# Optimization experiments

Measured on AMD Instinct MI355X. Metric: run time of the kernel, lower is better.

The kernel has to match this reference:

```python
import jax, jax.numpy as jnp
import numpy as np

EPS = 1e-5

def bn(x, g, b, m, v):
    # inference-mode BatchNorm2d over channel dim
    return (x - m[None, :, None, None]) * jax.lax.rsqrt(v[None, :, None, None] + EPS) * g[None, :, None, None] + b[None, :, None, None]

def conv1x1(x, W, b=None):
    y = jnp.einsum('oc,bchw->bohw', W, x)
    return y + b[None, :, None, None] if b is not None else y

def forward(x, W3, b3, g1, b1, m1, v1, Wa, ba, g2, b2, m2, v2, Wq, bq, Wk, bk, Wv, bv, gam, Wg, bg, g3, b3n, m3, v3, Wf, bf, g4, b4, m4, v4, Wr, rs):
    B, C, H, Wd = x.shape
    N = H * Wd
    # conv branch: 3x3 conv + BN + ReLU
    y3 = jax.lax.conv_general_dilated(x, W3, (1, 1), ((1, 1), (1, 1)), dimension_numbers=('NCHW', 'OIHW', 'NCHW'))
    local = jax.nn.relu(bn(y3 + b3[None, :, None, None], g1, b1, m1, v1))
    # attn branch: 1x1 conv + BN + ReLU, then full-resolution attention
    a = jax.nn.relu(bn(conv1x1(x, Wa, ba), g2, b2, m2, v2))
    q = conv1x1(a, Wq, bq).reshape(B, -1, N)   # [B, C/8, N]
    k = conv1x1(a, Wk, bk).reshape(B, -1, N)   # [B, C/8, N]
    v = conv1x1(a, Wv, bv).reshape(B, -1, N)   # [B, C, N]
    att = jax.nn.softmax(jnp.einsum('bcn,bcm->bnm', q, k), axis=-1)  # [B, N, N], unscaled as in source
    o = jnp.einsum('bcm,bnm->bcn', v, att).reshape(a.shape)
    attn_feat = gam * o + a
    # gated fusion
    combined = jnp.concatenate([local, attn_feat], axis=1)
    gate = jax.nn.sigmoid(bn(conv1x1(combined, Wg, bg), g3, b3n, m3, v3))
    fused = gate * local + (1.0 - gate) * attn_feat
    out = jax.nn.relu(bn(conv1x1(jnp.concatenate([fused, combined], axis=1), Wf, bf), g4, b4, m4, v4))
    res = conv1x1(x, Wr)  # residual 1x1 conv, no bias (in != out channels)
    return out + rs * res

def setup_inputs() -> dict:
    B, Ci, Co, H, W_ = 4, 64, 128, 64, 64
    Cq = Co // 8
    ks = jax.random.split(jax.random.key(0), 24)
    def rn(i, s, sc=0.05):
        return jax.random.normal(ks[i], s, jnp.float32) * sc
    def var(i, c):
        return jax.random.uniform(ks[i], (c,), jnp.float32, 0.5, 1.5)
    ones = lambda c: jnp.ones((c,), jnp.float32)
    zeros = lambda c: jnp.zeros((c,), jnp.float32)
    return {
        'x': rn(0, (B, Ci, H, W_), 1.0),
        'W3': rn(1, (Co, Ci, 3, 3)), 'b3': rn(2, (Co,)),
        'g1': ones(Co), 'b1': zeros(Co), 'm1': rn(3, (Co,), 0.1), 'v1': var(4, Co),
        'Wa': rn(5, (Co, Ci)), 'ba': rn(6, (Co,)),
        'g2': ones(Co), 'b2': zeros(Co), 'm2': rn(7, (Co,), 0.1), 'v2': var(8, Co),
        'Wq': rn(9, (Cq, Co)), 'bq': rn(10, (Cq,)),
        'Wk': rn(11, (Cq, Co)), 'bk': rn(12, (Cq,)),
        'Wv': rn(13, (Co, Co)), 'bv': rn(14, (Co,)),
        'gam': jnp.array(0.5, jnp.float32),
        'Wg': rn(15, (Co, 2 * Co)), 'bg': rn(16, (Co,)),
        'g3': ones(Co), 'b3n': zeros(Co), 'm3': rn(17, (Co,), 0.1), 'v3': var(18, Co),
        'Wf': rn(19, (Co, 3 * Co)), 'bf': rn(20, (Co,)),
        'g4': ones(Co), 'b4': zeros(Co), 'm4': rn(21, (Co,), 0.1), 'v4': var(22, Co),
        'Wr': rn(23, (Co, Ci)),
        'rs': jnp.array(0.1, jnp.float32),
    }

def reference(x, W3, b3, g1, b1, m1, v1, Wa, ba, g2, b2, m2, v2, Wq, bq, Wk, bk, Wv, bv, gam, Wg, bg, g3, b3n, m3, v3, Wf, bf, g4, b4, m4, v4, Wr, rs):
    return forward(x, W3, b3, g1, b1, m1, v1, Wa, ba, g2, b2, m2, v2, Wq, bq, Wk, bk, Wv, bv, gam, Wg, bg, g3, b3n, m3, v3, Wf, bf, g4, b4, m4, v4, Wr, rs)
```

## Files before the change

kernel.cpp:

```cpp
#include <hip/hip_runtime.h>
#include <hip/hip_bf16.h>

#define CI_ 64
#define CO_ 128
#define NPIX 4096
#define CQ_ 16
#define EPS_ 1e-5f

typedef __attribute__((ext_vector_type(8))) __bf16 bf16x8;
typedef __attribute__((ext_vector_type(4))) __bf16 bf16x4;
typedef __attribute__((ext_vector_type(4))) float f32x4;

__global__ __launch_bounds__(256) void z_prepx(
    const float* __restrict__ x, __bf16* __restrict__ xT)
{
    __shared__ float tl[64][65];
    int b = blockIdx.x >> 6;
    int n0 = (blockIdx.x & 63) * 64;
    int tid = threadIdx.x;
    int nn = tid & 63, c4 = tid >> 6;
#pragma unroll
    for (int p = 0; p < 16; ++p) {
        int ci = p * 4 + c4;
        tl[ci][nn] = x[((size_t)b * CI_ + ci) * NPIX + n0 + nn];
    }
    __syncthreads();
#pragma unroll
    for (int p = 0; p < 2; ++p) {
        int idx = p * 256 + tid;
        int n = idx >> 3, cig = idx & 7;
        bf16x8 vv;
#pragma unroll
        for (int j = 0; j < 8; ++j) vv[j] = (__bf16)tl[cig * 8 + j][n];
        ((bf16x8*)xT)[((size_t)b * NPIX + n0 + n) * 8 + cig] = vv;
    }
}

__global__ __launch_bounds__(256) void z_prepw2(
    const float* __restrict__ W3, __bf16* __restrict__ Wt2,
    const float* __restrict__ Wg, const float* __restrict__ Wf, const float* __restrict__ Wr,
    const float* __restrict__ Wa, const float* __restrict__ Wq, const float* __restrict__ Wk,
    const float* __restrict__ Wv, __bf16* __restrict__ Wb)
{
    int i = blockIdx.x * 256 + threadIdx.x;
    if (i < 73728) {
        int co = i / 576;
        int r = i - co * 576;
        int tap = r >> 6;
        int ci = r & 63;
        Wt2[i] = (__bf16)W3[((size_t)co * CI_ + ci) * 9 + tap];
    }
    if (i < 118784) {
        float val;
        if (i < 32768) val = Wg[i];
        else if (i < 81920) val = Wf[i - 32768];
        else if (i < 90112) val = Wr[i - 81920];
        else if (i < 98304) val = Wa[i - 90112];
        else if (i < 100352) val = Wq[i - 98304];
        else if (i < 102400) val = Wk[i - 100352];
        else val = Wv[i - 102400];
        Wb[i] = (__bf16)val;
    }
}

__global__ __launch_bounds__(256) void z_mega(
    const __bf16* __restrict__ xT, const __bf16* __restrict__ Wb,
    const float* __restrict__ ba, const float* __restrict__ g2, const float* __restrict__ b2,
    const float* __restrict__ m2, const float* __restrict__ v2,
    const float* __restrict__ bq, const float* __restrict__ bk, const float* __restrict__ bv,
    float* __restrict__ a, __bf16* __restrict__ qT, __bf16* __restrict__ kT, __bf16* __restrict__ V2)
{
    __shared__ __align__(16) __bf16 an[16 * 128];
    int tid = threadIdx.x;
    int b = blockIdx.x >> 8;
    int n0 = (blockIdx.x & 255) * 16;
    int l = tid & 63, w = tid >> 6;
    int lm = l & 15, g = l >> 4;

    const __bf16* Wa2 = Wb + 90112;
    const __bf16* Wq2 = Wb + 98304;
    const __bf16* Wk2 = Wb + 100352;
    const __bf16* Wv2 = Wb + 102400;

    bf16x8 bx[2];
#pragma unroll
    for (int kc = 0; kc < 2; ++kc)
        bx[kc] = ((const bf16x8*)xT)[((size_t)b * NPIX + n0 + lm) * 8 + (kc * 4 + g)];
    f32x4 pa[2];
#pragma unroll
    for (int ct = 0; ct < 2; ++ct) {
#pragma unroll
        for (int r = 0; r < 4; ++r) pa[ct][r] = ba[w * 32 + ct * 16 + g * 4 + r];
#pragma unroll
        for (int kc = 0; kc < 2; ++kc) {
            bf16x8 afr = *(const bf16x8*)&Wa2[(size_t)(w * 32 + ct * 16 + lm) * 64 + kc * 32 + g * 8];
            pa[ct] = __builtin_amdgcn_mfma_f32_16x16x32_bf16(afr, bx[kc], pa[ct], 0, 0, 0);
        }
    }
#pragma unroll
    for (int ct = 0; ct < 2; ++ct) {
        bf16x4 pk;
#pragma unroll
        for (int r = 0; r < 4; ++r) {
            int co = w * 32 + ct * 16 + g * 4 + r;
            float sc = rsqrtf(v2[co] + EPS_) * g2[co];
            float sh = b2[co] - m2[co] * sc;
            float y = fmaxf(pa[ct][r] * sc + sh, 0.f);
            a[((size_t)b * CO_ + co) * NPIX + n0 + lm] = y;
            pk[r] = (__bf16)y;
        }
        int co8 = w * 4 + ct * 2 + (g >> 1);
        int ch = co8 ^ (lm & 7);
        *(bf16x4*)&an[lm * 128 + ch * 8 + (g & 1) * 4] = pk;
    }
    __syncthreads();

    bf16x8 bn[4];
#pragma unroll
    for (int kc = 0; kc < 4; ++kc) {
        int ch = (kc * 4 + g) ^ (lm & 7);
        bn[kc] = *(const bf16x8*)&an[lm * 128 + ch * 8];
    }
    f32x4 pv[2];
#pragma unroll
    for (int ct = 0; ct < 2; ++ct) {
#pragma unroll
        for (int r = 0; r < 4; ++r) pv[ct][r] = bv[w * 32 + ct * 16 + g * 4 + r];
#pragma unroll
        for (int kc = 0; kc < 4; ++kc) {
            bf16x8 afr = *(const bf16x8*)&Wv2[(size_t)(w * 32 + ct * 16 + lm) * 128 + kc * 32 + g * 8];
            pv[ct] = __builtin_amdgcn_mfma_f32_16x16x32_bf16(afr, bn[kc], pv[ct], 0, 0, 0);
        }
    }
    int n = n0 + lm;
#pragma unroll
    for (int ct = 0; ct < 2; ++ct)
#pragma unroll
        for (int r = 0; r < 4; ++r) {
            int c = w * 32 + ct * 16 + g * 4 + r;
            V2[(size_t)b * 524288 + (size_t)(n >> 3) * 1024 + c * 8 + (n & 7)] = (__bf16)pv[ct][r];
        }
    if (w == 0) {
        f32x4 pq;
#pragma unroll
        for (int r = 0; r < 4; ++r) pq[r] = bq[g * 4 + r];
#pragma unroll
        for (int kc = 0; kc < 4; ++kc) {
            bf16x8 afr = *(const bf16x8*)&Wq2[(size_t)lm * 128 + kc * 32 + g * 8];
            pq = __builtin_amdgcn_mfma_f32_16x16x32_bf16(afr, bn[kc], pq, 0, 0, 0);
        }
        bf16x4 qq;
#pragma unroll
        for (int r = 0; r < 4; ++r) qq[r] = (__bf16)pq[r];
        *(bf16x4*)&qT[((size_t)b * NPIX + n) * CQ_ + g * 4] = qq;
    } else if (w == 1) {
        f32x4 pk2;
#pragma unroll
        for (int r = 0; r < 4; ++r) pk2[r] = bk[g * 4 + r];
#pragma unroll
        for (int kc = 0; kc < 4; ++kc) {
            bf16x8 afr = *(const bf16x8*)&Wk2[(size_t)lm * 128 + kc * 32 + g * 8];
            pk2 = __builtin_amdgcn_mfma_f32_16x16x32_bf16(afr, bn[kc], pk2, 0, 0, 0);
        }
        bf16x4 kk;
#pragma unroll
        for (int r = 0; r < 4; ++r) kk[r] = (__bf16)pk2[r];
        *(bf16x4*)&kT[((size_t)b * NPIX + n) * CQ_ + g * 4] = kk;
    }
}

__global__ __launch_bounds__(256) void z_conv3mb(
    const __bf16* __restrict__ xT, const __bf16* __restrict__ Wt2,
    const float* __restrict__ b3, const float* __restrict__ g,
    const float* __restrict__ bb, const float* __restrict__ m,
    const float* __restrict__ v, __bf16* __restrict__ local_bf)
{
    __shared__ __align__(16) __bf16 xt[3 * 66 * 64];
    __shared__ __align__(16) __bf16 wt[32 * 576];
    __shared__ float scs[32], shs[32];

    int blk = blockIdx.x;
    int b = blk >> 8;
    int h = (blk >> 2) & 63;
    int cg = blk & 3;
    int co0 = cg * 32;
    int tid = threadIdx.x;
    int l = tid & 63;
    int nt = tid >> 6;
    int lm = l & 15, lh = l >> 4;

    if (tid < 32) {
        int co = co0 + tid;
        float scv = rsqrtf(v[co] + EPS_) * g[co];
        scs[tid] = scv;
        shs[tid] = (b3[co] - m[co]) * scv + bb[co];
    }

    const bf16x8* xs = (const bf16x8*)xT + (size_t)b * (NPIX * 8);
    for (int i = tid; i < 1584; i += 256) {
        int r = i / 528;
        int rem = i - r * 528;
        int c = rem >> 3;
        int cig = rem & 7;
        int hh = h + r - 1;
        int gc = c - 1;
        bf16x8 val;
#pragma unroll
        for (int j = 0; j < 8; ++j) val[j] = (__bf16)0.f;
        if ((unsigned)hh < 64u && (unsigned)gc < 64u)
            val = xs[(hh * 64 + gc) * 8 + cig];
        *(bf16x8*)&xt[(r * 66 + c) * 64 + ((cig ^ (c & 7)) * 8)] = val;
    }
    const bf16x8* wsrc = (const bf16x8*)Wt2 + (size_t)co0 * 72;
    for (int i = tid; i < 2304; i += 256) {
        int co = i / 72;
        int kc = i - co * 72;
        *(bf16x8*)&wt[co * 576 + ((kc ^ (co & 7)) * 8)] = wsrc[i];
    }
    __syncthreads();

    f32x4 acc0 = {0.f, 0.f, 0.f, 0.f};
    f32x4 acc1 = {0.f, 0.f, 0.f, 0.f};
#pragma unroll
    for (int tap = 0; tap < 9; ++tap) {
        int dh = tap / 3, dw = tap % 3;
#pragma unroll
        for (int ks = 0; ks < 2; ++ks) {
            int cig = ks * 4 + lh;
            int col = nt * 16 + lm + dw;
            bf16x8 bfr = *(const bf16x8*)&xt[(dh * 66 + col) * 64 + ((cig ^ (col & 7)) * 8)];
            int kcg = tap * 8 + cig;
            bf16x8 a0 = *(const bf16x8*)&wt[lm * 576 + ((kcg ^ (lm & 7)) * 8)];
            bf16x8 a1 = *(const bf16x8*)&wt[(16 + lm) * 576 + ((kcg ^ (lm & 7)) * 8)];
            acc0 = __builtin_amdgcn_mfma_f32_16x16x32_bf16(a0, bfr, acc0, 0, 0, 0);
            acc1 = __builtin_amdgcn_mfma_f32_16x16x32_bf16(a1, bfr, acc1, 0, 0, 0);
        }
    }

    size_t obase = (size_t)b * CO_ * NPIX + h * 64 + nt * 16 + lm;
#pragma unroll
    for (int r = 0; r < 4; ++r) {
        int cl0 = lh * 4 + r;
        float y0 = fmaxf(acc0[r] * scs[cl0] + shs[cl0], 0.f);
        local_bf[obase + (size_t)(co0 + cl0) * NPIX] = (__bf16)y0;
        int cl1 = 16 + cl0;
        float y1 = fmaxf(acc1[r] * scs[cl1] + shs[cl1], 0.f);
        local_bf[obase + (size_t)(co0 + cl1) * NPIX] = (__bf16)y1;
    }
}

__global__ __launch_bounds__(256) void z_attn9(
    const __bf16* __restrict__ qT, const __bf16* __restrict__ kT, const __bf16* __restrict__ V2,
    __bf16* __restrict__ o_part, float2* __restrict__ ml)
{
    __shared__ __align__(16) unsigned char smem[16896];
    __shared__ float wredA[4][16], wredB[4][16];
    __bf16* pA = (__bf16*)smem;
    __bf16* pB = (__bf16*)(smem + 8448);
    float* o_lds = (float*)smem;

    int tid = threadIdx.x;
    int b = blockIdx.x >> 8;
    int half = (blockIdx.x >> 7) & 1;
    int q0 = (blockIdx.x & 127) * 32;
    int l = tid & 63;
    int w = tid >> 6;
    int lm = l & 15;
    int g = l >> 4;

    bf16x8 qfA, qfB;
#pragma unroll
    for (int j = 0; j < 8; ++j) { qfA[j] = (__bf16)0.f; qfB[j] = (__bf16)0.f; }
    const __bf16* qtb = qT + (size_t)b * NPIX * CQ_;
    if (g < 2) {
        qfA = *(const bf16x8*)&qtb[(size_t)(q0 + lm) * CQ_ + g * 8];
        qfB = *(const bf16x8*)&qtb[(size_t)(q0 + 16 + lm) * CQ_ + g * 8];
    }

    const bf16x8* vbase = (const bf16x8*)V2 + (size_t)b * 65536;
    const __bf16* ktb = kT + (size_t)b * NPIX * CQ_;

    float mxA = -1e30f, mxB = -1e30f;
    for (int t = 0; t < 8; ++t) {
        int m0 = half * 2048 + t * 256;
#pragma unroll
        for (int ms = 0; ms < 4; ++ms) {
            bf16x8 kf;
#pragma unroll
            for (int j = 0; j < 8; ++j) kf[j] = (__bf16)0.f;
            if (g < 2)
                kf = *(const bf16x8*)&ktb[(size_t)(m0 + w * 64 + ms * 16 + lm) * CQ_ + g * 8];
            f32x4 zz = {0.f, 0.f, 0.f, 0.f};
            f32x4 sA = __builtin_amdgcn_mfma_f32_16x16x32_bf16(kf, qfA, zz, 0, 0, 0);
            f32x4 sB = __builtin_amdgcn_mfma_f32_16x16x32_bf16(kf, qfB, zz, 0, 0, 0);
#pragma unroll
            for (int r = 0; r < 4; ++r) {
                mxA = fmaxf(mxA, sA[r]);
                mxB = fmaxf(mxB, sB[r]);
            }
        }
    }
    mxA = fmaxf(mxA, __shfl_xor(mxA, 16));
    mxA = fmaxf(mxA, __shfl_xor(mxA, 32));
    mxB = fmaxf(mxB, __shfl_xor(mxB, 16));
    mxB = fmaxf(mxB, __shfl_xor(mxB, 32));
    if (g == 0) { wredA[w][lm] = mxA; wredB[w][lm] = mxB; }
    __syncthreads();
    float MA = fmaxf(fmaxf(wredA[0][lm], wredA[1][lm]), fmaxf(wredA[2][lm], wredA[3][lm]));
    float MB = fmaxf(fmaxf(wredB[0][lm], wredB[1][lm]), fmaxf(wredB[2][lm], wredB[3][lm]));

    f32x4 aA0 = {0.f,0.f,0.f,0.f}, aA1 = {0.f,0.f,0.f,0.f};
    f32x4 aB0 = {0.f,0.f,0.f,0.f}, aB1 = {0.f,0.f,0.f,0.f};
    float sumA = 0.f, sumB = 0.f;
    int c0 = w * 32 + lm;
    int c1 = c0 + 16;

    for (int t = 0; t < 8; ++t) {
        int m0 = half * 2048 + t * 256;
#pragma unroll
        for (int ms = 0; ms < 4; ++ms) {
            bf16x8 kf;
#pragma unroll
            for (int j = 0; j < 8; ++j) kf[j] = (__bf16)0.f;
            if (g < 2)
                kf = *(const bf16x8*)&ktb[(size_t)(m0 + w * 64 + ms * 16 + lm) * CQ_ + g * 8];
            f32x4 zz = {0.f, 0.f, 0.f, 0.f};
            f32x4 sA = __builtin_amdgcn_mfma_f32_16x16x32_bf16(kf, qfA, zz, 0, 0, 0);
            f32x4 sB = __builtin_amdgcn_mfma_f32_16x16x32_bf16(kf, qfB, zz, 0, 0, 0);
            float a0 = __expf(sA[0] - MA), a1 = __expf(sA[1] - MA);
            float a2 = __expf(sA[2] - MA), a3 = __expf(sA[3] - MA);
            sumA += (a0 + a1) + (a2 + a3);
            bf16x4 pkA;
            pkA[0] = (__bf16)a0; pkA[1] = (__bf16)a1; pkA[2] = (__bf16)a2; pkA[3] = (__bf16)a3;
            *(bf16x4*)&pA[lm * 264 + w * 64 + ms * 16 + g * 4] = pkA;
            float b0 = __expf(sB[0] - MB), b1 = __expf(sB[1] - MB);
            float b2 = __expf(sB[2] - MB), b3 = __expf(sB[3] - MB);
            sumB += (b0 + b1) + (b2 + b3);
            bf16x4 pkB;
            pkB[0] = (__bf16)b0; pkB[1] = (__bf16)b1; pkB[2] = (__bf16)b2; pkB[3] = (__bf16)b3;
            *(bf16x4*)&pB[lm * 264 + w * 64 + ms * 16 + g * 4] = pkB;
        }
        __syncthreads();
#pragma unroll
        for (int ks = 0; ks < 8; ++ks) {
            int msv = (m0 >> 3) + ks * 4 + g;
            bf16x8 bf0 = vbase[msv * 128 + c0];
            bf16x8 bf1 = vbase[msv * 128 + c1];
            bf16x8 afA = *(const bf16x8*)&pA[lm * 264 + ks * 32 + g * 8];
            bf16x8 afB = *(const bf16x8*)&pB[lm * 264 + ks * 32 + g * 8];
            aA0 = __builtin_amdgcn_mfma_f32_16x16x32_bf16(afA, bf0, aA0, 0, 0, 0);
            aA1 = __builtin_amdgcn_mfma_f32_16x16x32_bf16(afA, bf1, aA1, 0, 0, 0);
            aB0 = __builtin_amdgcn_mfma_f32_16x16x32_bf16(afB, bf0, aB0, 0, 0, 0);
            aB1 = __builtin_amdgcn_mfma_f32_16x16x32_bf16(afB, bf1, aB1, 0, 0, 0);
        }
        __syncthreads();
    }

    sumA += __shfl_xor(sumA, 16);
    sumA += __shfl_xor(sumA, 32);
    sumB += __shfl_xor(sumB, 16);
    sumB += __shfl_xor(sumB, 32);
    if (g == 0) { wredA[w][lm] = sumA; wredB[w][lm] = sumB; }
    __syncthreads();
    float lA = (wredA[0][lm] + wredA[1][lm]) + (wredA[2][lm] + wredA[3][lm]);
    float lB = (wredB[0][lm] + wredB[1][lm]) + (wredB[2][lm] + wredB[3][lm]);

#pragma unroll
    for (int r = 0; r < 4; ++r) {
        int qrow = g * 4 + r;
        o_lds[c0 * 17 + qrow] = aA0[r];
        o_lds[c1 * 17 + qrow] = aA1[r];
    }
    if (w == 0 && g == 0)
        ml[(size_t)(half * 4 + b) * NPIX + q0 + lm] = make_float2(MA, lA);
    __syncthreads();
    {
        int qi = tid & 15;
        float inv = 1.f / lA;
#pragma unroll
        for (int j = 0; j < 8; ++j) {
            int cc = (tid >> 4) + 16 * j;
            size_t idx = ((size_t)(half * 4 + b) * CO_ + cc) * NPIX + q0 + qi;
            o_part[idx] = (__bf16)(o_lds[cc * 17 + qi] * inv);
        }
    }
    __syncthreads();
#pragma unroll
    for (int r = 0; r < 4; ++r) {
        int qrow = g * 4 + r;
        o_lds[c0 * 17 + qrow] = aB0[r];
        o_lds[c1 * 17 + qrow] = aB1[r];
    }
    if (w == 0 && g == 0)
        ml[(size_t)(half * 4 + b) * NPIX + q0 + 16 + lm] = make_float2(MB, lB);
    __syncthreads();
    {
        int qi = tid & 15;
        float inv = 1.f / lB;
#pragma unroll
        for (int j = 0; j < 8; ++j) {
            int cc = (tid >> 4) + 16 * j;
            size_t idx = ((size_t)(half * 4 + b) * CO_ + cc) * NPIX + q0 + 16 + qi;
            o_part[idx] = (__bf16)(o_lds[cc * 17 + qi] * inv);
        }
    }
}

__global__ __launch_bounds__(256) void z_fuseout3(
    const __bf16* __restrict__ local_bf, const __bf16* __restrict__ o_part,
    const float2* __restrict__ ml, const float* __restrict__ a,
    const float* __restrict__ gamp, const __bf16* __restrict__ xT,
    const __bf16* __restrict__ Wb,
    const float* __restrict__ bg, const float* __restrict__ g3, const float* __restrict__ b3n,
    const float* __restrict__ m3, const float* __restrict__ v3,
    const float* __restrict__ bfb, const float* __restrict__ g4, const float* __restrict__ b4,
    const float* __restrict__ m4, const float* __restrict__ v4,
    const float* __restrict__ rsp, float* __restrict__ out)
{
    __shared__ __align__(16) unsigned char smem[32768 + 4096];
    __shared__ float wA[32], wB[32];
    __bf16* sb2 = (__bf16*)smem;
    __bf16* sxT = (__bf16*)(smem + 28672);

    int tid = threadIdx.x;
    int b = blockIdx.x >> 7;
    int n0 = (blockIdx.x & 127) * 32;

    if (tid < 32) {
        float2 m1 = ml[(size_t)b * NPIX + n0 + tid];
        float2 m2 = ml[(size_t)(4 + b) * NPIX + n0 + tid];
        float mm = fmaxf(m1.x, m2.x);
        float w1 = m1.y * __expf(m1.x - mm);
        float w2 = m2.y * __expf(m2.x - mm);
        float inv = 1.f / (w1 + w2);
        wA[tid] = w1 * inv;
        wB[tid] = w2 * inv;
    }
    __syncthreads();

    float gam = gamp[0];
#pragma unroll
    for (int p = 0; p < 4; ++p) {
        int idx = p * 256 + tid;
        int c = idx >> 3, j = idx & 7;
        bf16x4 lv = *(const bf16x4*)&local_bf[((size_t)b * CO_ + c) * NPIX + n0 + j * 4];
        bf16x4 o1 = *(const bf16x4*)&o_part[((size_t)b * CO_ + c) * NPIX + n0 + j * 4];
        bf16x4 o2 = *(const bf16x4*)&o_part[((size_t)(4 + b) * CO_ + c) * NPIX + n0 + j * 4];
        float av[4];
        *(float4*)av = *(const float4*)(a + ((size_t)b * CO_ + c) * NPIX + n0 + j * 4);
#pragma unroll
        for (int e = 0; e < 4; ++e) {
            int n = j * 4 + e;
            int k1 = 128 + c, k2 = 256 + c;
            sb2[n * 448 + (((k1 >> 3) ^ (n & 7)) << 3) + (k1 & 7)] = lv[e];
            float o = (float)o1[e] * wA[n] + (float)o2[e] * wB[n];
            sb2[n * 448 + (((k2 >> 3) ^ (n & 7)) << 3) + (k2 & 7)] = (__bf16)(gam * o + av[e]);
        }
    }
#pragma unroll
    for (int p = 0; p < 2; ++p) {
        int idx = p * 256 + tid;
        int n = idx >> 3, cig = idx & 7;
        bf16x8 vv = ((const bf16x8*)xT)[((size_t)b * NPIX + n0 + n) * 8 + cig];
        *(bf16x8*)&sxT[n * 64 + ((cig ^ (n & 7)) << 3)] = vv;
    }
    __syncthreads();

    int l = tid & 63, w = tid >> 6;
    int lm = l & 15, g = l >> 4;
    int co0 = w * 32;
    int t7 = lm & 7;

    f32x4 p1[2][2];
#pragma unroll
    for (int cs = 0; cs < 2; ++cs) {
        float bv = bg[co0 + cs * 16 + lm];
#pragma unroll
        for (int ns = 0; ns < 2; ++ns) {
            p1[ns][cs][0] = bv; p1[ns][cs][1] = bv; p1[ns][cs][2] = bv; p1[ns][cs][3] = bv;
        }
    }
    const __bf16* Wg2 = Wb;
#pragma unroll
    for (int kc = 0; kc < 8; ++kc) {
        int ch = (16 + kc * 4 + g) ^ t7;
        bf16x8 a0 = *(const bf16x8*)&sb2[lm * 448 + ch * 8];
        bf16x8 a1 = *(const bf16x8*)&sb2[(16 + lm) * 448 + ch * 8];
        bf16x8 b0 = *(const bf16x8*)&Wg2[(size_t)(co0 + lm) * 256 + kc * 32 + g * 8];
        bf16x8 b1 = *(const bf16x8*)&Wg2[(size_t)(co0 + 16 + lm) * 256 + kc * 32 + g * 8];
        p1[0][0] = __builtin_amdgcn_mfma_f32_16x16x32_bf16(a0, b0, p1[0][0], 0, 0, 0);
        p1[0][1] = __builtin_amdgcn_mfma_f32_16x16x32_bf16(a0, b1, p1[0][1], 0, 0, 0);
        p1[1][0] = __builtin_amdgcn_mfma_f32_16x16x32_bf16(a1, b0, p1[1][0], 0, 0, 0);
        p1[1][1] = __builtin_amdgcn_mfma_f32_16x16x32_bf16(a1, b1, p1[1][1], 0, 0, 0);
    }
#pragma unroll
    for (int cs = 0; cs < 2; ++cs) {
        int co = co0 + cs * 16 + lm;
        float sc3 = rsqrtf(v3[co] + EPS_) * g3[co];
        float sh3 = b3n[co] - m3[co] * sc3;
        int kl = 128 + co, ka = 256 + co;
#pragma unroll
        for (int ns = 0; ns < 2; ++ns)
#pragma unroll
            for (int r = 0; r < 4; ++r) {
                int n = ns * 16 + g * 4 + r;
                float z = p1[ns][cs][r] * sc3 + sh3;
                float gate = 1.f / (1.f + __expf(-z));
                float lv = (float)sb2[n * 448 + (((kl >> 3) ^ (n & 7)) << 3) + (kl & 7)];
                float av = (float)sb2[n * 448 + (((ka >> 3) ^ (n & 7)) << 3) + (ka & 7)];
                float fu = gate * lv + (1.f - gate) * av;
                sb2[n * 448 + (((co >> 3) ^ (n & 7)) << 3) + (co & 7)] = (__bf16)fu;
            }
    }
    __syncthreads();

    f32x4 p2[2][2], pr[2][2];
#pragma unroll
    for (int cs = 0; cs < 2; ++cs) {
        float bv = bfb[co0 + cs * 16 + lm];
#pragma unroll
        for (int ns = 0; ns < 2; ++ns) {
            p2[ns][cs][0] = bv; p2[ns][cs][1] = bv; p2[ns][cs][2] = bv; p2[ns][cs][3] = bv;
            pr[ns][cs] = (f32x4){0.f, 0.f, 0.f, 0.f};
        }
    }
    const __bf16* Wf2 = Wb + 32768;
    const __bf16* Wr2 = Wb + 81920;
#pragma unroll
    for (int kc = 0; kc < 12; ++kc) {
        int ch = (kc * 4 + g) ^ t7;
        bf16x8 a0 = *(const bf16x8*)&sb2[lm * 448 + ch * 8];
        bf16x8 a1 = *(const bf16x8*)&sb2[(16 + lm) * 448 + ch * 8];
        bf16x8 b0 = *(const bf16x8*)&Wf2[(size_t)(co0 + lm) * 384 + kc * 32 + g * 8];
        bf16x8 b1 = *(const bf16x8*)&Wf2[(size_t)(co0 + 16 + lm) * 384 + kc * 32 + g * 8];
        p2[0][0] = __builtin_amdgcn_mfma_f32_16x16x32_bf16(a0, b0, p2[0][0], 0, 0, 0);
        p2[0][1] = __builtin_amdgcn_mfma_f32_16x16x32_bf16(a0, b1, p2[0][1], 0, 0, 0);
        p2[1][0] = __builtin_amdgcn_mfma_f32_16x16x32_bf16(a1, b0, p2[1][0], 0, 0, 0);
        p2[1][1] = __builtin_amdgcn_mfma_f32_16x16x32_bf16(a1, b1, p2[1][1], 0, 0, 0);
    }
#pragma unroll
    for (int kc = 0; kc < 2; ++kc) {
        int ch = (kc * 4 + g) ^ t7;
        bf16x8 a0 = *(const bf16x8*)&sxT[lm * 64 + ch * 8];
        bf16x8 a1 = *(const bf16x8*)&sxT[(16 + lm) * 64 + ch * 8];
        bf16x8 b0 = *(const bf16x8*)&Wr2[(size_t)(co0 + lm) * 64 + kc * 32 + g * 8];
        bf16x8 b1 = *(const bf16x8*)&Wr2[(size_t)(co0 + 16 + lm) * 64 + kc * 32 + g * 8];
        pr[0][0] = __builtin_amdgcn_mfma_f32_16x16x32_bf16(a0, b0, pr[0][0], 0, 0, 0);
        pr[0][1] = __builtin_amdgcn_mfma_f32_16x16x32_bf16(a0, b1, pr[0][1], 0, 0, 0);
        pr[1][0] = __builtin_amdgcn_mfma_f32_16x16x32_bf16(a1, b0, pr[1][0], 0, 0, 0);
        pr[1][1] = __builtin_amdgcn_mfma_f32_16x16x32_bf16(a1, b1, pr[1][1], 0, 0, 0);
    }
    __syncthreads();

    float* o_lds = (float*)smem;
    float rsv = rsp[0];
#pragma unroll
    for (int cs = 0; cs < 2; ++cs) {
        int co = co0 + cs * 16 + lm;
        float sc4 = rsqrtf(v4[co] + EPS_) * g4[co];
        float sh4 = b4[co] - m4[co] * sc4;
#pragma unroll
        for (int ns = 0; ns < 2; ++ns)
#pragma unroll
            for (int r = 0; r < 4; ++r) {
                int n = ns * 16 + g * 4 + r;
                float o = fmaxf(p2[ns][cs][r] * sc4 + sh4, 0.f) + rsv * pr[ns][cs][r];
                o_lds[co * 36 + n] = o;
            }
    }
    __syncthreads();
    {
        int c = tid >> 1, h = tid & 1;
#pragma unroll
        for (int j2 = 0; j2 < 4; ++j2) {
            float4 vv = *(float4*)&o_lds[c * 36 + h * 16 + j2 * 4];
            *(float4*)(out + ((size_t)b * CO_ + c) * NPIX + n0 + h * 16 + j2 * 4) = vv;
        }
    }
}

extern "C" void kernel_launch(void* const* d_in, const int* in_sizes, int n_in,
                              void* d_out, int out_size, void* d_ws, size_t ws_size,
                              hipStream_t stream) {
    const float* x   = (const float*)d_in[0];
    const float* W3  = (const float*)d_in[1];
    const float* b3  = (const float*)d_in[2];
    const float* g1  = (const float*)d_in[3];
    const float* b1  = (const float*)d_in[4];
    const float* m1  = (const float*)d_in[5];
    const float* v1  = (const float*)d_in[6];
    const float* Wa  = (const float*)d_in[7];
    const float* ba  = (const float*)d_in[8];
    const float* g2  = (const float*)d_in[9];
    const float* b2  = (const float*)d_in[10];
    const float* m2  = (const float*)d_in[11];
    const float* v2  = (const float*)d_in[12];
    const float* Wq  = (const float*)d_in[13];
    const float* bq  = (const float*)d_in[14];
    const float* Wk  = (const float*)d_in[15];
    const float* bk  = (const float*)d_in[16];
    const float* Wv  = (const float*)d_in[17];
    const float* bv  = (const float*)d_in[18];
    const float* gam = (const float*)d_in[19];
    const float* Wg  = (const float*)d_in[20];
    const float* bg  = (const float*)d_in[21];
    const float* g3  = (const float*)d_in[22];
    const float* b3n = (const float*)d_in[23];
    const float* m3  = (const float*)d_in[24];
    const float* v3  = (const float*)d_in[25];
    const float* Wf  = (const float*)d_in[26];
    const float* bfb = (const float*)d_in[27];
    const float* g4  = (const float*)d_in[28];
    const float* b4  = (const float*)d_in[29];
    const float* m4  = (const float*)d_in[30];
    const float* v4  = (const float*)d_in[31];
    const float* Wr  = (const float*)d_in[32];
    const float* rs  = (const float*)d_in[33];

    float* ws      = (float*)d_ws;
    float* a_      = ws;
    __bf16* local_bf = (__bf16*)(ws + 2097152);
    __bf16* V2     = (__bf16*)(ws + 3145728);
    __bf16* qT     = (__bf16*)(ws + 4194304);
    __bf16* kT     = (__bf16*)(ws + 4325376);
    __bf16* xT     = (__bf16*)(ws + 4456448);
    __bf16* Wt2    = (__bf16*)(ws + 4980736);
    __bf16* Wb     = (__bf16*)(ws + 5017600);
    __bf16* o_part = (__bf16*)(ws + 5076992);
    float2* ml     = (float2*)(ws + 7174144);

    float* out = (float*)d_out;

    z_prepx<<<256, 256, 0, stream>>>(x, xT);
    z_prepw2<<<464, 256, 0, stream>>>(W3, Wt2, Wg, Wf, Wr, Wa, Wq, Wk, Wv, Wb);
    z_mega<<<1024, 256, 0, stream>>>(xT, Wb, ba, g2, b2, m2, v2, bq, bk, bv, a_, qT, kT, V2);
    z_attn9<<<1024, 256, 0, stream>>>(qT, kT, V2, o_part, ml);
    z_conv3mb<<<1024, 256, 0, stream>>>(xT, Wt2, b3, g1, b1, m1, v1, local_bf);
    z_fuseout3<<<512, 256, 0, stream>>>(local_bf, o_part, ml, a_, gam, xT, Wb,
                                        bg, g3, b3n, m3, v3, bfb, g4, b4, m4, v4, rs, out);
}
```

Baseline: 106.5 us.

## Replace softmax max pre-pass with Cauchy-Schwarz bound from query and key norms

The attention kernel no longer runs a first pass over all keys to find the exact row maximum of the scores. Instead, the projection kernel records each batch's largest squared key norm with an atomic max, and the attention kernel uses sqrt(|q|^2 * max|k|^2) as the softmax shift. This removes a full sweep of key loads, MFMAs and a block reduction per query tile. Any shift gives the same softmax, but a loose bound can push exponentials toward underflow when query and key norms are large. It also adds an atomic per output group in the projection kernel.

```diff
diff --git a/kernel.cpp b/kernel.cpp
--- a/kernel.cpp
+++ b/kernel.cpp
@@ -40,9 +40,10 @@
     const float* __restrict__ W3, __bf16* __restrict__ Wt2,
     const float* __restrict__ Wg, const float* __restrict__ Wf, const float* __restrict__ Wr,
     const float* __restrict__ Wa, const float* __restrict__ Wq, const float* __restrict__ Wk,
-    const float* __restrict__ Wv, __bf16* __restrict__ Wb)
+    const float* __restrict__ Wv, __bf16* __restrict__ Wb, float* __restrict__ kmax2)
 {
     int i = blockIdx.x * 256 + threadIdx.x;
+    if (i < 4) ((unsigned int*)kmax2)[i] = 0u;
     if (i < 73728) {
         int co = i / 576;
         int r = i - co * 576;
@@ -68,7 +69,8 @@
     const float* __restrict__ ba, const float* __restrict__ g2, const float* __restrict__ b2,
     const float* __restrict__ m2, const float* __restrict__ v2,
     const float* __restrict__ bq, const float* __restrict__ bk, const float* __restrict__ bv,
-    float* __restrict__ a, __bf16* __restrict__ qT, __bf16* __restrict__ kT, __bf16* __restrict__ V2)
+    float* __restrict__ a, __bf16* __restrict__ qT, __bf16* __restrict__ kT,
+    __bf16* __restrict__ V2, float* __restrict__ kmax2)
 {
     __shared__ __align__(16) __bf16 an[16 * 128];
     int tid = threadIdx.x;
@@ -166,6 +168,11 @@
 #pragma unroll
         for (int r = 0; r < 4; ++r) kk[r] = (__bf16)pk2[r];
         *(bf16x4*)&kT[((size_t)b * NPIX + n) * CQ_ + g * 4] = kk;
+        float kn2 = pk2[0]*pk2[0] + pk2[1]*pk2[1] + pk2[2]*pk2[2] + pk2[3]*pk2[3];
+        kn2 += __shfl_xor(kn2, 16);
+        kn2 += __shfl_xor(kn2, 32);
+        if (g == 0)
+            atomicMax((unsigned int*)&kmax2[b], __float_as_uint(kn2));
     }
 }
 
@@ -249,9 +256,9 @@
     }
 }
 
-__global__ __launch_bounds__(256) void z_attn9(
+__global__ __launch_bounds__(256) void z_attn11(
     const __bf16* __restrict__ qT, const __bf16* __restrict__ kT, const __bf16* __restrict__ V2,
-    __bf16* __restrict__ o_part, float2* __restrict__ ml)
+    const float* __restrict__ kmax2, __bf16* __restrict__ o_part, float2* __restrict__ ml)
 {
     __shared__ __align__(16) unsigned char smem[16896];
     __shared__ float wredA[4][16], wredB[4][16];
@@ -277,37 +284,20 @@
         qfB = *(const bf16x8*)&qtb[(size_t)(q0 + 16 + lm) * CQ_ + g * 8];
     }
 
+    float qa2 = 0.f, qb2 = 0.f;
+#pragma unroll
+    for (int j = 0; j < 8; ++j) {
+        qa2 += (float)qfA[j] * (float)qfA[j];
+        qb2 += (float)qfB[j] * (float)qfB[j];
+    }
+    qa2 += __shfl_xor(qa2, 16); qa2 += __shfl_xor(qa2, 32);
+    qb2 += __shfl_xor(qb2, 16); qb2 += __shfl_xor(qb2, 32);
+    float km = kmax2[b];
+    float MA = sqrtf(qa2 * km);
+    float MB = sqrtf(qb2 * km);
+
     const bf16x8* vbase = (const bf16x8*)V2 + (size_t)b * 65536;
     const __bf16* ktb = kT + (size_t)b * NPIX * CQ_;
-
-    float mxA = -1e30f, mxB = -1e30f;
-    for (int t = 0; t < 8; ++t) {
-        int m0 = half * 2048 + t * 256;
-#pragma unroll
-        for (int ms = 0; ms < 4; ++ms) {
-            bf16x8 kf;
-#pragma unroll
-            for (int j = 0; j < 8; ++j) kf[j] = (__bf16)0.f;
-            if (g < 2)
-                kf = *(const bf16x8*)&ktb[(size_t)(m0 + w * 64 + ms * 16 + lm) * CQ_ + g * 8];
-            f32x4 zz = {0.f, 0.f, 0.f, 0.f};
-            f32x4 sA = __builtin_amdgcn_mfma_f32_16x16x32_bf16(kf, qfA, zz, 0, 0, 0);
-            f32x4 sB = __builtin_amdgcn_mfma_f32_16x16x32_bf16(kf, qfB, zz, 0, 0, 0);
-#pragma unroll
-            for (int r = 0; r < 4; ++r) {
-                mxA = fmaxf(mxA, sA[r]);
-                mxB = fmaxf(mxB, sB[r]);
-            }
-        }
-    }
-    mxA = fmaxf(mxA, __shfl_xor(mxA, 16));
-    mxA = fmaxf(mxA, __shfl_xor(mxA, 32));
-    mxB = fmaxf(mxB, __shfl_xor(mxB, 16));
-    mxB = fmaxf(mxB, __shfl_xor(mxB, 32));
-    if (g == 0) { wredA[w][lm] = mxA; wredB[w][lm] = mxB; }
-    __syncthreads();
-    float MA = fmaxf(fmaxf(wredA[0][lm], wredA[1][lm]), fmaxf(wredA[2][lm], wredA[3][lm]));
-    float MB = fmaxf(fmaxf(wredB[0][lm], wredB[1][lm]), fmaxf(wredB[2][lm], wredB[3][lm]));
 
     f32x4 aA0 = {0.f,0.f,0.f,0.f}, aA1 = {0.f,0.f,0.f,0.f};
     f32x4 aB0 = {0.f,0.f,0.f,0.f}, aB1 = {0.f,0.f,0.f,0.f};
@@ -628,13 +618,14 @@
     __bf16* Wb     = (__bf16*)(ws + 5017600);
     __bf16* o_part = (__bf16*)(ws + 5076992);
     float2* ml     = (float2*)(ws + 7174144);
+    float* kmax2   = ws + 7239680;
 
     float* out = (float*)d_out;
 
     z_prepx<<<256, 256, 0, stream>>>(x, xT);
-    z_prepw2<<<464, 256, 0, stream>>>(W3, Wt2, Wg, Wf, Wr, Wa, Wq, Wk, Wv, Wb);
-    z_mega<<<1024, 256, 0, stream>>>(xT, Wb, ba, g2, b2, m2, v2, bq, bk, bv, a_, qT, kT, V2);
-    z_attn9<<<1024, 256, 0, stream>>>(qT, kT, V2, o_part, ml);
+    z_prepw2<<<464, 256, 0, stream>>>(W3, Wt2, Wg, Wf, Wr, Wa, Wq, Wk, Wv, Wb, kmax2);
+    z_mega<<<1024, 256, 0, stream>>>(xT, Wb, ba, g2, b2, m2, v2, bq, bk, bv, a_, qT, kT, V2, kmax2);
+    z_attn11<<<1024, 256, 0, stream>>>(qT, kT, V2, kmax2, o_part, ml);
     z_conv3mb<<<1024, 256, 0, stream>>>(xT, Wt2, b3, g1, b1, m1, v1, local_bf);
     z_fuseout3<<<512, 256, 0, stream>>>(local_bf, o_part, ml, a_, gam, xT, Wb,
                                         bg, g3, b3n, m3, v3, bfb, g4, b4, m4, v4, rs, out);
```

New measurement: 109.3 us. 2.6% more time.
